# Performance work log

Hardware: AMD Instinct MI355X
Metric: run time of the kernel (lower is better)

Reference implementation:

```python
import jax, jax.numpy as jnp
import numpy as np

TEMPERATURE = 0.1
EPS = 1e-12  # torch F.normalize eps

N, H, NUM_CLASSES = 8192, 1024, 64


def setup_inputs() -> dict:
    key = jax.random.key(0)
    k1, k2 = jax.random.split(key)
    utter_emb = jax.random.normal(k1, (N, H), dtype=jnp.float32)
    labels = jax.random.randint(k2, (N,), 0, NUM_CLASSES, dtype=jnp.int64)
    return {"utter_emb": utter_emb, "labels": labels}


def reference(utter_emb, labels):
    # Normalize rows -> cosine similarity matrix. (normalize + cosine_similarity
    # of already-normalized vectors == plain cosine sim of raw vectors.)
    norms = jnp.maximum(jnp.linalg.norm(utter_emb, axis=1, keepdims=True), EPS)
    x = utter_emb / norms                              # (N, H)
    sim = x @ x.T                                      # (N, N) cosine sims
    e = jnp.exp(sim / TEMPERATURE)                     # (N, N)

    n = utter_emb.shape[0]
    not_self = ~jnp.eye(n, dtype=bool)                 # exclude i itself
    pos_mask = (labels[:, None] == labels[None, :]) & not_self

    pos_cnt = pos_mask.sum(axis=1)                     # (N,)
    # numerator: mean over positives of exp(sim/T)
    numerator = (e * pos_mask).sum(axis=1) / jnp.maximum(pos_cnt, 1)
    # denominator: sum over ALL j != i (original neg_keys includes positives)
    denominator = (e * not_self).sum(axis=1)

    per_sample = -(jnp.log(numerator) - jnp.log(denominator))
    valid = pos_cnt > 0                                # only samples with >=1 positive
    count = valid.sum()
    cl_loss = jnp.where(valid, per_sample, 0.0).sum() / count
    return cl_loss
```

## Files before the change

kernel.cpp:

```cpp
#include <hip/hip_runtime.h>
#include <hip/hip_bf16.h>

#define N_ROWS 8192
#define H_DIM  1024
#define NUM_CLS 64
#define BM 128
#define BN 128
#define NBLK (N_ROWS / BM)
#define KSTRIDE ((size_t)N_ROWS * 16)
#define SCALE_E8M0 0x79797979
#define FIX2 1048576.0f
#define FIXSCALE 16777216.0
#define GRID_K2 (8 * 264)
#define NFIN 32

typedef float f32x4 __attribute__((ext_vector_type(4)));
typedef int   i32x4 __attribute__((ext_vector_type(4)));
typedef int   i32x8 __attribute__((ext_vector_type(8)));
typedef unsigned long long u64;

__device__ __forceinline__ float fast_exp2(float x) {
    float r;
    asm("v_exp_f32 %0, %1" : "=v"(r) : "v"(x));
    return r;
}

__device__ __forceinline__ unsigned enc_fp4(float f) {
    const float a = fabsf(f);
    unsigned c = (unsigned)(a > 0.25f) + (unsigned)(a > 0.75f) +
                 (unsigned)(a > 1.25f) + (unsigned)(a > 1.75f) +
                 (unsigned)(a > 2.5f)  + (unsigned)(a > 3.5f) +
                 (unsigned)(a > 5.0f);
    return c | ((__float_as_uint(f) >> 31) << 3);
}

__global__ __launch_bounds__(256) void norm_kernel(const float* __restrict__ in,
                                                   unsigned char* __restrict__ xqT,
                                                   const int* __restrict__ labels,
                                                   int* __restrict__ ghist,
                                                   u64* __restrict__ rsum_pos,
                                                   u64* __restrict__ rsum_all) {
    if (threadIdx.x < 16) {
        const int r0 = blockIdx.x * 16 + threadIdx.x;
        rsum_pos[r0] = 0ULL;
        rsum_all[r0] = 0ULL;
        atomicAdd(&ghist[labels[r0]], 1);
    }
    __shared__ __align__(16) unsigned char lt[16 * 528];
    const int tid  = threadIdx.x;
    const int wid  = tid >> 6, lane = tid & 63;
    const int r = lane >> 4, c = lane & 15;
    const int lrow = wid * 4 + r;
    const int row  = blockIdx.x * 16 + lrow;
    const float4* src = reinterpret_cast<const float4*>(in + (size_t)row * H_DIM)
                        + c * 16;
    float4 v[16];
    float ss = 0.f;
#pragma unroll
    for (int i = 0; i < 16; ++i) {
        v[i] = src[i];
        ss += v[i].x * v[i].x + v[i].y * v[i].y + v[i].z * v[i].z + v[i].w * v[i].w;
    }
#pragma unroll
    for (int d = 1; d < 16; d <<= 1) ss += __shfl_xor(ss, d, 64);
    const float inv = 64.0f / fmaxf(sqrtf(ss), 1e-12f);
#pragma unroll
    for (int h = 0; h < 2; ++h) {
        i32x4 dw;
#pragma unroll
        for (int j = 0; j < 4; ++j) {
            unsigned d = 0;
#pragma unroll
            for (int k = 0; k < 8; ++k) {
                const int e = j * 8 + k;
                const float f = ((const float*)&v[h * 8 + (e >> 2)])[e & 3] * inv;
                d |= enc_fp4(f) << (4 * k);
            }
            dw[j] = (int)d;
        }
        *reinterpret_cast<i32x4*>(&lt[lrow * 528 + (2 * c + h) * 16]) = dw;
    }
    __syncthreads();
#pragma unroll
    for (int it = 0; it < 2; ++it) {
        const int p  = it * 16 + (tid >> 4);
        const int rr = tid & 15;
        *reinterpret_cast<i32x4*>(xqT + (size_t)p * KSTRIDE +
                                  (size_t)(blockIdx.x * 16 + rr) * 16) =
            *reinterpret_cast<const i32x4*>(&lt[rr * 528 + p * 16]);
    }
}

__device__ __constant__ unsigned char OFF_TBL[28] = {
    1, 2, 3, 4, 5, 6, 7,
    10, 11, 12, 13, 14, 15,
    19, 20, 21, 22, 23,
    28, 29, 30, 31,
    37, 38, 39,
    46, 47,
    55
};

__global__ __launch_bounds__(256)
void simloss_kernel(const unsigned char* __restrict__ xqT, const int* __restrict__ labels,
                    u64* __restrict__ rsum_pos, u64* __restrict__ rsum_all) {
    __shared__ float sc[1024];

    const int xcd = blockIdx.x & 7;
    const int n   = blockIdx.x >> 3;
    int I, J;
    if (xcd < 4) {
        if (n >= 256) return;
        const int t = OFF_TBL[xcd * 4 + (n >> 6)];
        I = (t >> 3) * 8 + ((n >> 3) & 7);
        J = (t & 7) * 8 + (n & 7);
    } else if (n < 192) {
        const int t = OFF_TBL[16 + (xcd - 4) * 3 + (n >> 6)];
        I = (t >> 3) * 8 + ((n >> 3) & 7);
        J = (t & 7) * 8 + (n & 7);
    } else {
        int n2 = n - 192;
        const int D = (xcd - 4) * 2 + (n2 >= 36 ? 1 : 0);
        int t2 = (n2 >= 36) ? n2 - 36 : n2;
        int i = 0;
        while (t2 >= 8 - i) { t2 -= 8 - i; ++i; }
        I = D * 8 + i;
        J = D * 8 + i + t2;
    }
    const bool diag = (I == J);
    const int row0 = I * BM, col0 = J * BN;

    const int tid  = threadIdx.x;
    const int lane = tid & 63;
    const int wid  = tid >> 6;
    const int wr = wid >> 1, wc = wid & 1;
    const int l15 = lane & 15, lq = lane >> 4;

    f32x4 acc[4][4];
#pragma unroll
    for (int m = 0; m < 4; ++m)
#pragma unroll
        for (int n2 = 0; n2 < 4; ++n2) acc[m][n2] = (f32x4){0.f, 0.f, 0.f, 0.f};

    const unsigned char* Ap = xqT + (size_t)lq * KSTRIDE + (size_t)(row0 + wr * 64 + l15) * 16;
    const unsigned char* Bp = xqT + (size_t)lq * KSTRIDE + (size_t)(col0 + wc * 64 + l15) * 16;
    const i32x4 z4 = {0, 0, 0, 0};

#define LOADS(BUF, S)                                                          \
    do {                                                                       \
        _Pragma("unroll")                                                      \
        for (int m = 0; m < 4; ++m)                                            \
            A##BUF[m] = *reinterpret_cast<const i32x4*>(                       \
                Ap + (size_t)(S) * 4 * KSTRIDE + m * 256);                     \
        _Pragma("unroll")                                                      \
        for (int n2 = 0; n2 < 4; ++n2)                                         \
            B##BUF[n2] = *reinterpret_cast<const i32x4*>(                      \
                Bp + (size_t)(S) * 4 * KSTRIDE + n2 * 256);                    \
    } while (0)

#define MFMA_STEP(BUF)                                                         \
    do {                                                                       \
        __builtin_amdgcn_s_setprio(1);                                         \
        _Pragma("unroll")                                                      \
        for (int m = 0; m < 4; ++m) {                                          \
            const i32x8 a8 = __builtin_shufflevector(A##BUF[m], z4,            \
                                                     0, 1, 2, 3, 4, 5, 6, 7);  \
            _Pragma("unroll")                                                  \
            for (int n2 = 0; n2 < 4; ++n2) {                                   \
                const i32x8 b8 = __builtin_shufflevector(B##BUF[n2], z4,       \
                                                         0, 1, 2, 3, 4, 5, 6, 7); \
                acc[m][n2] = __builtin_amdgcn_mfma_scale_f32_16x16x128_f8f6f4( \
                    a8, b8, acc[m][n2], 4, 4, 0, SCALE_E8M0, 0, SCALE_E8M0);   \
            }                                                                  \
        }                                                                      \
        __builtin_amdgcn_s_setprio(0);                                         \
    } while (0)

    i32x4 A0[4], B0[4], A1[4], B1[4], A2[4], B2[4];
    LOADS(0, 0);
    LOADS(1, 1);
    LOADS(2, 2);
    MFMA_STEP(0);
    LOADS(0, 3);
    MFMA_STEP(1);
    LOADS(1, 4);
    MFMA_STEP(2);
    LOADS(2, 5);
    MFMA_STEP(0);
    LOADS(0, 6);
    MFMA_STEP(1);
    LOADS(1, 7);
    MFMA_STEP(2);
    MFMA_STEP(0);
    MFMA_STEP(1);
#undef LOADS
#undef MFMA_STEP

    int lab_r[16];
#pragma unroll
    for (int m = 0; m < 4; ++m)
#pragma unroll
        for (int r = 0; r < 4; ++r)
            lab_r[m * 4 + r] = labels[row0 + wr * 64 + m * 16 + lq * 4 + r];

    float rs_pos[16], rs_all[16];
#pragma unroll
    for (int i = 0; i < 16; ++i) { rs_pos[i] = 0.f; rs_all[i] = 0.f; }
    float cs_pos[4], cs_all[4];
#pragma unroll
    for (int n2 = 0; n2 < 4; ++n2) { cs_pos[n2] = 0.f; cs_all[n2] = 0.f; }

#pragma unroll
    for (int n2 = 0; n2 < 4; ++n2) {
        const int colg = col0 + wc * 64 + n2 * 16 + l15;
        const int lab_c = labels[colg];
#pragma unroll
        for (int m = 0; m < 4; ++m) {
#pragma unroll
            for (int r = 0; r < 4; ++r) {
                const int rowg = row0 + wr * 64 + m * 16 + lq * 4 + r;
                const float e = fast_exp2(acc[m][n2][r] * 14.4269504088896340736f);
                const bool self = (rowg == colg);
                const bool pos  = (lab_c == lab_r[m * 4 + r]) && !self;
                const float ea = self ? 0.f : e;
                const float ep = pos ? e : 0.f;
                rs_all[m * 4 + r] += ea;
                rs_pos[m * 4 + r] += ep;
                cs_all[n2] += ea;
                cs_pos[n2] += ep;
            }
        }
    }

#pragma unroll
    for (int i = 0; i < 16; ++i) {
#pragma unroll
        for (int d = 1; d < 16; d <<= 1) {
            rs_pos[i] += __shfl_xor(rs_pos[i], d, 64);
            rs_all[i] += __shfl_xor(rs_all[i], d, 64);
        }
    }
#pragma unroll
    for (int n2 = 0; n2 < 4; ++n2) {
#pragma unroll
        for (int d = 16; d < 64; d <<= 1) {
            cs_pos[n2] += __shfl_xor(cs_pos[n2], d, 64);
            cs_all[n2] += __shfl_xor(cs_all[n2], d, 64);
        }
    }

    float* rowpos = sc;
    float* rowall = sc + 256;
    float* colpos = sc + 512;
    float* colall = sc + 768;
    if (l15 == 0) {
#pragma unroll
        for (int i = 0; i < 16; ++i) {
            const int m = i >> 2, r = i & 3;
            const int lr = wr * 64 + m * 16 + lq * 4 + r;
            rowpos[wc * 128 + lr] = rs_pos[i];
            rowall[wc * 128 + lr] = rs_all[i];
        }
    }
    if (lq == 0 && !diag) {
#pragma unroll
        for (int n2 = 0; n2 < 4; ++n2) {
            const int lc = wc * 64 + n2 * 16 + l15;
            colpos[wr * 128 + lc] = cs_pos[n2];
            colall[wr * 128 + lc] = cs_all[n2];
        }
    }
    __syncthreads();

    if (tid < 128) {
        const float rp = rowpos[tid] + rowpos[128 + tid];
        const float ra = rowall[tid] + rowall[128 + tid];
        atomicAdd(&rsum_pos[row0 + tid], (u64)(rp * FIX2 + 0.5f));
        atomicAdd(&rsum_all[row0 + tid], (u64)(ra * FIX2 + 0.5f));
    } else if (!diag) {
        const int t2 = tid - 128;
        const float cp = colpos[t2] + colpos[128 + t2];
        const float ca = colall[t2] + colall[128 + t2];
        atomicAdd(&rsum_pos[col0 + t2], (u64)(cp * FIX2 + 0.5f));
        atomicAdd(&rsum_all[col0 + t2], (u64)(ca * FIX2 + 0.5f));
    }
}

__global__ __launch_bounds__(256)
void finalize_kernel(const int* __restrict__ labels, const u64* __restrict__ rsum_pos,
                     const u64* __restrict__ rsum_all, const int* __restrict__ ghist,
                     u64* __restrict__ acc, float* __restrict__ out) {
    __shared__ float sred[4];
    __shared__ int scnt[4];
    const int tid = threadIdx.x;
    const int i = blockIdx.x * 256 + tid;

    const u64 rp = rsum_pos[i];
    const u64 ra = rsum_all[i];
    const int cnt = ghist[labels[i]] - 1;
    float lsum = 0.f;
    int vcnt = 0;
    if (cnt > 0) {
        const float p = fmaxf((float)((double)rp / (double)FIX2), 1e-30f);
        const float a = (float)((double)ra / (double)FIX2);
        lsum = logf(a) - logf(p) + logf((float)cnt);
        vcnt = 1;
    }
    const int lane = tid & 63, wid = tid >> 6;
#pragma unroll
    for (int d = 1; d < 64; d <<= 1) {
        lsum += __shfl_xor(lsum, d, 64);
        vcnt += __shfl_xor(vcnt, d, 64);
    }
    if (lane == 0) { sred[wid] = lsum; scnt[wid] = vcnt; }
    __syncthreads();
    if (tid == 0) {
        const double bs = (double)(sred[0] + sred[1] + sred[2] + sred[3]);
        const u64 S = (u64)(bs * FIXSCALE + 0.5);
        const u64 C = (u64)(scnt[0] + scnt[1] + scnt[2] + scnt[3]);
        atomicAdd(&acc[1], S);
        atomicAdd(&acc[2], C);
        __threadfence();
        const u64 tk = atomicAdd(&acc[0], 1ULL);
        if (tk == (u64)(NFIN - 1)) {
            volatile u64* va = acc;
            const double St = (double)va[1];
            const double Ct = (double)va[2];
            out[0] = (float)(St / FIXSCALE / Ct);
        }
    }
}

extern "C" void kernel_launch(void* const* d_in, const int* in_sizes, int n_in,
                              void* d_out, int out_size, void* d_ws, size_t ws_size,
                              hipStream_t stream) {
    const float* emb   = (const float*)d_in[0];
    const int* labels  = (const int*)d_in[1];
    float* out         = (float*)d_out;
    char* ws           = (char*)d_ws;

    unsigned char* xqT = (unsigned char*)ws;
    u64* rsum_pos = (u64*)(ws + (size_t)32 * KSTRIDE);
    u64* rsum_all = rsum_pos + N_ROWS;
    u64* acc      = rsum_all + N_ROWS;
    int* ghist    = (int*)(acc + 4);

    hipMemsetAsync(acc, 0, 4 * sizeof(u64) + NUM_CLS * sizeof(int), stream);
    norm_kernel<<<N_ROWS / 16, 256, 0, stream>>>(emb, xqT, labels, ghist,
                                                 rsum_pos, rsum_all);
    simloss_kernel<<<GRID_K2, 256, 0, stream>>>(xqT, labels, rsum_pos, rsum_all);
    finalize_kernel<<<NFIN, 256, 0, stream>>>(labels, rsum_pos, rsum_all, ghist,
                                              acc, out);
}
```

Measured before the change: 73.30 us.

## Drop memset launch, build label histogram in finalize, double-buffer MFMA loads

```diff
diff --git a/kernel.cpp b/kernel.cpp
--- a/kernel.cpp
+++ b/kernel.cpp
@@ -36,15 +36,14 @@
 
 __global__ __launch_bounds__(256) void norm_kernel(const float* __restrict__ in,
                                                    unsigned char* __restrict__ xqT,
-                                                   const int* __restrict__ labels,
-                                                   int* __restrict__ ghist,
                                                    u64* __restrict__ rsum_pos,
-                                                   u64* __restrict__ rsum_all) {
+                                                   u64* __restrict__ rsum_all,
+                                                   u64* __restrict__ acc) {
+    if (blockIdx.x == 0 && threadIdx.x < 4) acc[threadIdx.x] = 0ULL;
     if (threadIdx.x < 16) {
         const int r0 = blockIdx.x * 16 + threadIdx.x;
         rsum_pos[r0] = 0ULL;
         rsum_all[r0] = 0ULL;
-        atomicAdd(&ghist[labels[r0]], 1);
     }
     __shared__ __align__(16) unsigned char lt[16 * 528];
     const int tid  = threadIdx.x;
@@ -144,7 +143,6 @@
 
     const unsigned char* Ap = xqT + (size_t)lq * KSTRIDE + (size_t)(row0 + wr * 64 + l15) * 16;
     const unsigned char* Bp = xqT + (size_t)lq * KSTRIDE + (size_t)(col0 + wc * 64 + l15) * 16;
-    const i32x4 z4 = {0, 0, 0, 0};
 
 #define LOADS(BUF, S)                                                          \
     do {                                                                       \
@@ -158,43 +156,45 @@
                 Bp + (size_t)(S) * 4 * KSTRIDE + n2 * 256);                    \
     } while (0)
 
-#define MFMA_STEP(BUF)                                                         \
+#define BUILD8(dst, src) (dst) = __builtin_shufflevector((src), (src),         \
+                                                         0, 1, 2, 3, -1, -1, -1, -1)
+
+#define STEP(CUR, NXT, S, LAST)                                                \
     do {                                                                       \
+        if (!(LAST)) LOADS(NXT, (S) + 1);                                      \
+        i32x8 b80, b81, b82, b83;                                              \
+        BUILD8(b80, B##CUR[0]); BUILD8(b81, B##CUR[1]);                        \
+        BUILD8(b82, B##CUR[2]); BUILD8(b83, B##CUR[3]);                        \
         __builtin_amdgcn_s_setprio(1);                                         \
         _Pragma("unroll")                                                      \
         for (int m = 0; m < 4; ++m) {                                          \
-            const i32x8 a8 = __builtin_shufflevector(A##BUF[m], z4,            \
-                                                     0, 1, 2, 3, 4, 5, 6, 7);  \
-            _Pragma("unroll")                                                  \
-            for (int n2 = 0; n2 < 4; ++n2) {                                   \
-                const i32x8 b8 = __builtin_shufflevector(B##BUF[n2], z4,       \
-                                                         0, 1, 2, 3, 4, 5, 6, 7); \
-                acc[m][n2] = __builtin_amdgcn_mfma_scale_f32_16x16x128_f8f6f4( \
-                    a8, b8, acc[m][n2], 4, 4, 0, SCALE_E8M0, 0, SCALE_E8M0);   \
-            }                                                                  \
+            i32x8 a8;                                                          \
+            BUILD8(a8, A##CUR[m]);                                             \
+            acc[m][0] = __builtin_amdgcn_mfma_scale_f32_16x16x128_f8f6f4(      \
+                a8, b80, acc[m][0], 4, 4, 0, SCALE_E8M0, 0, SCALE_E8M0);       \
+            acc[m][1] = __builtin_amdgcn_mfma_scale_f32_16x16x128_f8f6f4(      \
+                a8, b81, acc[m][1], 4, 4, 0, SCALE_E8M0, 0, SCALE_E8M0);       \
+            acc[m][2] = __builtin_amdgcn_mfma_scale_f32_16x16x128_f8f6f4(      \
+                a8, b82, acc[m][2], 4, 4, 0, SCALE_E8M0, 0, SCALE_E8M0);       \
+            acc[m][3] = __builtin_amdgcn_mfma_scale_f32_16x16x128_f8f6f4(      \
+                a8, b83, acc[m][3], 4, 4, 0, SCALE_E8M0, 0, SCALE_E8M0);       \
         }                                                                      \
         __builtin_amdgcn_s_setprio(0);                                         \
     } while (0)
 
-    i32x4 A0[4], B0[4], A1[4], B1[4], A2[4], B2[4];
+    i32x4 A0[4], B0[4], A1[4], B1[4];
     LOADS(0, 0);
-    LOADS(1, 1);
-    LOADS(2, 2);
-    MFMA_STEP(0);
-    LOADS(0, 3);
-    MFMA_STEP(1);
-    LOADS(1, 4);
-    MFMA_STEP(2);
-    LOADS(2, 5);
-    MFMA_STEP(0);
-    LOADS(0, 6);
-    MFMA_STEP(1);
-    LOADS(1, 7);
-    MFMA_STEP(2);
-    MFMA_STEP(0);
-    MFMA_STEP(1);
+    STEP(0, 1, 0, false);
+    STEP(1, 0, 1, false);
+    STEP(0, 1, 2, false);
+    STEP(1, 0, 3, false);
+    STEP(0, 1, 4, false);
+    STEP(1, 0, 5, false);
+    STEP(0, 1, 6, false);
+    STEP(1, 0, 7, true);
 #undef LOADS
-#undef MFMA_STEP
+#undef BUILD8
+#undef STEP
 
     int lab_r[16];
 #pragma unroll
@@ -288,16 +288,21 @@
 
 __global__ __launch_bounds__(256)
 void finalize_kernel(const int* __restrict__ labels, const u64* __restrict__ rsum_pos,
-                     const u64* __restrict__ rsum_all, const int* __restrict__ ghist,
-                     u64* __restrict__ acc, float* __restrict__ out) {
+                     const u64* __restrict__ rsum_all, u64* __restrict__ acc,
+                     float* __restrict__ out) {
+    __shared__ int hist[NUM_CLS];
     __shared__ float sred[4];
     __shared__ int scnt[4];
     const int tid = threadIdx.x;
+    if (tid < NUM_CLS) hist[tid] = 0;
+    __syncthreads();
+    for (int i = tid; i < N_ROWS; i += 256) atomicAdd(&hist[labels[i]], 1);
+    __syncthreads();
+
     const int i = blockIdx.x * 256 + tid;
-
     const u64 rp = rsum_pos[i];
     const u64 ra = rsum_all[i];
-    const int cnt = ghist[labels[i]] - 1;
+    const int cnt = hist[labels[i]] - 1;
     float lsum = 0.f;
     int vcnt = 0;
     if (cnt > 0) {
@@ -343,12 +348,8 @@
     u64* rsum_pos = (u64*)(ws + (size_t)32 * KSTRIDE);
     u64* rsum_all = rsum_pos + N_ROWS;
     u64* acc      = rsum_all + N_ROWS;
-    int* ghist    = (int*)(acc + 4);
-
-    hipMemsetAsync(acc, 0, 4 * sizeof(u64) + NUM_CLS * sizeof(int), stream);
-    norm_kernel<<<N_ROWS / 16, 256, 0, stream>>>(emb, xqT, labels, ghist,
-                                                 rsum_pos, rsum_all);
+
+    norm_kernel<<<N_ROWS / 16, 256, 0, stream>>>(emb, xqT, rsum_pos, rsum_all, acc);
     simloss_kernel<<<GRID_K2, 256, 0, stream>>>(xqT, labels, rsum_pos, rsum_all);
-    finalize_kernel<<<NFIN, 256, 0, stream>>>(labels, rsum_pos, rsum_all, ghist,
-                                              acc, out);
-}
+    finalize_kernel<<<NFIN, 256, 0, stream>>>(labels, rsum_pos, rsum_all, acc, out);
+}
```

Measured after the change: 64.62 us. 1.13x faster.
